# Kernel optimization log

Measured on AMD Instinct MI355X. Metric: run time of the kernel, lower is better.

## Reference

```python
import jax, jax.numpy as jnp
import numpy as np

B, NUM, TC, H = 64, 8, 64, 128
STD = 0.1


def setup_inputs() -> dict:
    key = jax.random.key(0)
    ks = jax.random.split(key, 7)
    return {
        "x": jax.random.normal(ks[0], (B, NUM, TC, H), jnp.float32),
        "att_v": jax.random.normal(ks[1], (TC, 1), jnp.float32) * STD,
        "att_w": jax.random.normal(ks[2], (H, TC), jnp.float32) * STD,
        "att_u": jax.random.normal(ks[3], (TC, TC), jnp.float32) * STD,
        "gru_kernel": jax.random.normal(ks[4], (H, 3 * H), jnp.float32) * STD,
        "gru_rkernel": jax.random.normal(ks[5], (H, 3 * H), jnp.float32) * STD,
        "gru_bias": jnp.zeros((2, 3 * H), jnp.float32),
    }


def _attention_gru(x, att_v, att_w, att_u, gru_kernel, gru_rkernel, gru_bias):
    # x: [B, num, Tc, H]. Each of the `num` attribute groups runs an independent
    # recurrence, so fold num into the batch dimension (vectorizes the outer
    # Python loop of the original).
    b, num, tc, h = x.shape
    bn = b * num
    attr = x.transpose(0, 1, 3, 2).reshape(bn, h, tc)          # [BN, H, Tc]
    # attr_input[:, i] @ u is time-invariant: hoist out of the t-loop.
    uproj = jnp.einsum('bht,ts->bhs', attr, att_u)             # [BN, H, Tc]
    v = att_v[:, 0]                                            # [Tc]
    xs = attr.transpose(2, 0, 1)                               # [Tc, BN, H]
    b_in, b_rec = gru_bias[0], gru_bias[1]                      # reset_after biases

    def step(h_state, x_col):
        # DA-RNN input attention: e_i = v^T tanh(W h + U x_i) per hidden unit i
        h_part = h_state @ att_w                               # [BN, Tc]
        e = jnp.einsum('bht,t->bh', jnp.tanh(h_part[:, None, :] + uproj), v)
        a = jax.nn.softmax(e, axis=-1)                         # [BN, H]
        x_t = x_col * a                                        # matmul-with-diag == elementwise
        # Keras GRUCell, activation=relu, recurrent_activation=sigmoid, reset_after=True
        xm = x_t @ gru_kernel + b_in                           # [BN, 3H]
        rm = h_state @ gru_rkernel + b_rec                     # [BN, 3H]
        xz, xr, xh = jnp.split(xm, 3, axis=-1)
        rz, rr, rh = jnp.split(rm, 3, axis=-1)
        z = jax.nn.sigmoid(xz + rz)
        r = jax.nn.sigmoid(xr + rr)
        hh = jax.nn.relu(xh + r * rh)
        h_new = z * h_state + (1.0 - z) * hh
        return h_new, None

    h0 = jnp.zeros((bn, h), x.dtype)
    h_final, _ = jax.lax.scan(step, h0, xs)
    return h_final.reshape(b, num, h)                          # [B, num, H]


def reference(x, att_v, att_w, att_u, gru_kernel, gru_rkernel, gru_bias):
    return _attention_gru(x, att_v, att_w, att_u, gru_kernel, gru_rkernel, gru_bias)
```

## Files before the change

kernel.cpp:

```cpp
#include <hip/hip_runtime.h>


#define OFF_ATTW  0
#define OFF_U     8192
#define OFF_XMRM  12288
#define OFF_HST   13824
#define OFF_HPP   14080
#define OFF_HPART 14592
#define OFF_XTV   14720
#define OFF_VV    14976
#define OFF_RED   15040
#define LDS_FLOATS 15056

#define FMA4(ACC, W, S) do { (ACC).x += (W).x*(S); (ACC).y += (W).y*(S); \
                             (ACC).z += (W).z*(S); (ACC).w += (W).w*(S); } while(0)

__global__ __launch_bounds__(256, 1)
void attn_gru_kernel(const float* __restrict__ x, const float* __restrict__ att_v,
                     const float* __restrict__ att_w, const float* __restrict__ att_u,
                     const float* __restrict__ gk, const float* __restrict__ grk,
                     const float* __restrict__ gbias, float* __restrict__ out) {
    __shared__ float lds[LDS_FLOATS];
    const int tid = threadIdx.x;
    const int bn0 = blockIdx.x * 2;

    for (int i = tid; i < 8192; i += 256) lds[OFF_ATTW + i] = att_w[i];
    for (int i = tid; i < 4096; i += 256) lds[OFF_U + i] = att_u[i];
    if (tid < 64) lds[OFF_VV + tid] = att_v[tid];
    lds[OFF_HST + tid] = 0.0f;
    __syncthreads();

    const int seq = tid >> 7;
    const int hh  = tid & 127;
    const int s_  = tid & 63;
    const int hg  = tid >> 6;

    float upreg[64];
    #pragma unroll
    for (int s2 = 0; s2 < 64; ++s2) upreg[s2] = 0.0f;
    {
        const float* xb = x + (size_t)(bn0 + seq) * 8192 + hh;
        for (int t = 0; t < 64; ++t) {
            float xv = xb[t * 128];
            const float* Ur = lds + OFF_U + t * 64;
            #pragma unroll
            for (int s2 = 0; s2 < 64; ++s2) upreg[s2] += xv * Ur[s2];
        }
    }

    const int col4 = tid * 4;
    const int dmat = (col4 >= 384) ? 1 : 0;
    const int dj   = col4 - dmat * 384;
    const float* Wm = (dmat ? grk : gk) + dj;
    const int ivoff = dmat ? OFF_HST : OFF_XTV;
    float4 dbias = make_float4(0.f, 0.f, 0.f, 0.f);
    if (tid < 192) dbias = *(const float4*)(gbias + dmat * 384 + dj);

    const float* xcol = x + (size_t)(bn0 + seq) * 8192 + hh;

    __syncthreads();

    for (int t = 0; t < 64; ++t) {
        float xv = xcol[t * 128];

        {
            float p0 = 0.f, p1 = 0.f;
            const float* wgl = lds + OFF_ATTW + hg * 32 * 64 + s_;
            #pragma unroll
            for (int k = 0; k < 32; ++k) {
                float w = wgl[k * 64];
                p0 += lds[OFF_HST + hg * 32 + k] * w;
                p1 += lds[OFF_HST + 128 + hg * 32 + k] * w;
            }
            lds[OFF_HPP + (0 * 4 + hg) * 64 + s_] = p0;
            lds[OFF_HPP + (1 * 4 + hg) * 64 + s_] = p1;
        }
        __syncthreads();

        if (tid < 128) {
            int sq = tid >> 6, ss = tid & 63;
            lds[OFF_HPART + sq * 64 + ss] =
                  lds[OFF_HPP + (sq * 4 + 0) * 64 + ss]
                + lds[OFF_HPP + (sq * 4 + 1) * 64 + ss]
                + lds[OFF_HPP + (sq * 4 + 2) * 64 + ss]
                + lds[OFF_HPP + (sq * 4 + 3) * 64 + ss];
        }
        __syncthreads();

        float e = 0.f;
        {
            const float* hp = lds + OFF_HPART + seq * 64;
            #pragma unroll
            for (int s2 = 0; s2 < 64; ++s2) {
                float arg = hp[s2] + upreg[s2];
                float u2 = __expf(2.0f * arg);
                float th = 1.0f - __fdividef(2.0f, u2 + 1.0f);
                e += th * lds[OFF_VV + s2];
            }
        }
        float p = __expf(e);
        float sm = p;
        #pragma unroll
        for (int off = 32; off >= 1; off >>= 1) sm += __shfl_xor(sm, off, 64);
        if ((tid & 63) == 0) lds[OFF_RED + 8 + hg] = sm;
        __syncthreads();
        float denom = lds[OFF_RED + 8 + seq * 2] + lds[OFF_RED + 8 + seq * 2 + 1];
        float a = __fdividef(p, denom);
        lds[OFF_XTV + seq * 128 + hh] = a * xv;
        __syncthreads();

        if (tid < 192) {
            float4 a0 = make_float4(0.f, 0.f, 0.f, 0.f);
            float4 a1 = make_float4(0.f, 0.f, 0.f, 0.f);
            #pragma unroll 1
            for (int c = 0; c < 4; ++c) {
                float4 w[32];
                #pragma unroll
                for (int r = 0; r < 32; ++r)
                    w[r] = *(const float4*)(Wm + (size_t)(c * 32 + r) * 384);
                const float* i0 = lds + ivoff + c * 32;
                #pragma unroll
                for (int r4 = 0; r4 < 8; ++r4) {
                    float4 iA = *(const float4*)(i0 + r4 * 4);
                    float4 iB = *(const float4*)(i0 + 128 + r4 * 4);
                    FMA4(a0, w[r4*4+0], iA.x); FMA4(a1, w[r4*4+0], iB.x);
                    FMA4(a0, w[r4*4+1], iA.y); FMA4(a1, w[r4*4+1], iB.y);
                    FMA4(a0, w[r4*4+2], iA.z); FMA4(a1, w[r4*4+2], iB.z);
                    FMA4(a0, w[r4*4+3], iA.w); FMA4(a1, w[r4*4+3], iB.w);
                }
            }
            *(float4*)(lds + OFF_XMRM + (dmat * 2 + 0) * 384 + dj) =
                make_float4(a0.x + dbias.x, a0.y + dbias.y, a0.z + dbias.z, a0.w + dbias.w);
            *(float4*)(lds + OFF_XMRM + (dmat * 2 + 1) * 384 + dj) =
                make_float4(a1.x + dbias.x, a1.y + dbias.y, a1.z + dbias.z, a1.w + dbias.w);
        }
        __syncthreads();

        {
            const float* xm = lds + OFF_XMRM + (0 * 2 + seq) * 384;
            const float* rm = lds + OFF_XMRM + (1 * 2 + seq) * 384;
            float xz = xm[hh], xr = xm[128 + hh], xh = xm[256 + hh];
            float rz = rm[hh], rr = rm[128 + hh], rh = rm[256 + hh];
            float z = __fdividef(1.0f, 1.0f + __expf(-(xz + rz)));
            float r = __fdividef(1.0f, 1.0f + __expf(-(xr + rr)));
            float hc = xh + r * rh;
            hc = hc > 0.f ? hc : 0.f;
            float hold = lds[OFF_HST + seq * 128 + hh];
            lds[OFF_HST + seq * 128 + hh] = z * hold + (1.0f - z) * hc;
        }
        __syncthreads();
    }

    out[(size_t)(bn0 + seq) * 128 + hh] = lds[OFF_HST + seq * 128 + hh];
}

extern "C" void kernel_launch(void* const* d_in, const int* in_sizes, int n_in,
                              void* d_out, int out_size, void* d_ws, size_t ws_size,
                              hipStream_t stream) {
    (void)in_sizes; (void)n_in; (void)out_size; (void)d_ws; (void)ws_size;
    const float* x      = (const float*)d_in[0];
    const float* att_v  = (const float*)d_in[1];
    const float* att_w  = (const float*)d_in[2];
    const float* att_u  = (const float*)d_in[3];
    const float* gk     = (const float*)d_in[4];
    const float* grk    = (const float*)d_in[5];
    const float* gbias  = (const float*)d_in[6];
    float* out = (float*)d_out;
    hipLaunchKernelGGL(attn_gru_kernel, dim3(256), dim3(256), 0, stream,
                       x, att_v, att_w, att_u, gk, grk, gbias, out);
}
```

Baseline: 461.7 us.

## Process four sequences per block and restructure per-step work split

Each block now handles four batch-sequences instead of two, halving the grid to 128 blocks and amortising each global load of the GRU weights over four input vectors. The GRU matvec is remapped so all 256 threads compute three output columns each (previously only 192 threads were active). The attention projection drops the partial-sum reduction stage and its barrier, with one wave computing a full h·W row per sequence. The tanh-weighted sum is rewritten algebraically as sum(v) minus twice a weighted sum of 1/(exp+1). The cost is twice as many upreg registers per thread and only half as many blocks, so fewer CUs have work on a 256-CU part.

Result: slower. 789.7 us (+71.0%).

```diff
diff --git a/kernel.cpp b/kernel.cpp
--- a/kernel.cpp
+++ b/kernel.cpp
@@ -4,16 +4,15 @@
 #define OFF_ATTW  0
 #define OFF_U     8192
 #define OFF_XMRM  12288
-#define OFF_HST   13824
-#define OFF_HPP   14080
-#define OFF_HPART 14592
-#define OFF_XTV   14720
-#define OFF_VV    14976
-#define OFF_RED   15040
-#define LDS_FLOATS 15056
+#define OFF_HST   15360
+#define OFF_HPART 15872
+#define OFF_XTV   16128
+#define OFF_VV    16640
+#define OFF_RED   16704
+#define LDS_FLOATS 22016
 
-#define FMA4(ACC, W, S) do { (ACC).x += (W).x*(S); (ACC).y += (W).y*(S); \
-                             (ACC).z += (W).z*(S); (ACC).w += (W).w*(S); } while(0)
+#define FMA3(ACC, W, S) do { (ACC).x += (W).x*(S); (ACC).y += (W).y*(S); \
+                             (ACC).z += (W).z*(S); } while(0)
 
 __global__ __launch_bounds__(256, 1)
 void attn_gru_kernel(const float* __restrict__ x, const float* __restrict__ att_v,
@@ -22,136 +21,158 @@
                      const float* __restrict__ gbias, float* __restrict__ out) {
     __shared__ float lds[LDS_FLOATS];
     const int tid = threadIdx.x;
-    const int bn0 = blockIdx.x * 2;
+    const int bn0 = blockIdx.x * 4;
 
     for (int i = tid; i < 8192; i += 256) lds[OFF_ATTW + i] = att_w[i];
     for (int i = tid; i < 4096; i += 256) lds[OFF_U + i] = att_u[i];
     if (tid < 64) lds[OFF_VV + tid] = att_v[tid];
     lds[OFF_HST + tid] = 0.0f;
+    lds[OFF_HST + 256 + tid] = 0.0f;
     __syncthreads();
 
-    const int seq = tid >> 7;
-    const int hh  = tid & 127;
-    const int s_  = tid & 63;
-    const int hg  = tid >> 6;
+    const int c2  = tid >> 7;
+    const int chh = tid & 127;
+    const int w_  = tid >> 6;
+    const int asq = w_;
+    const int as_ = tid & 63;
+    const int dmat = (tid >= 128) ? 1 : 0;
+    const int dc   = 3 * (tid & 127);
+    const float* Wm = (dmat ? grk : gk) + dc;
+    const int din   = dmat ? OFF_HST : OFF_XTV;
+    const float3 b3 = *(const float3*)(gbias + dmat * 384 + dc);
 
-    float upreg[64];
+    float up0[64], up1[64];
     #pragma unroll
-    for (int s2 = 0; s2 < 64; ++s2) upreg[s2] = 0.0f;
+    for (int s2 = 0; s2 < 64; ++s2) { up0[s2] = 0.0f; up1[s2] = 0.0f; }
     {
-        const float* xb = x + (size_t)(bn0 + seq) * 8192 + hh;
+        const float* xb0 = x + (size_t)(bn0 + c2) * 8192 + chh;
+        const float* xb1 = x + (size_t)(bn0 + c2 + 2) * 8192 + chh;
         for (int t = 0; t < 64; ++t) {
-            float xv = xb[t * 128];
+            float xv0 = xb0[t * 128];
+            float xv1 = xb1[t * 128];
             const float* Ur = lds + OFF_U + t * 64;
             #pragma unroll
-            for (int s2 = 0; s2 < 64; ++s2) upreg[s2] += xv * Ur[s2];
+            for (int s2 = 0; s2 < 64; ++s2) {
+                float u = Ur[s2];
+                up0[s2] += xv0 * u;
+                up1[s2] += xv1 * u;
+            }
         }
     }
+    float sv = 0.0f;
+    #pragma unroll
+    for (int s2 = 0; s2 < 64; ++s2) sv += lds[OFF_VV + s2];
 
-    const int col4 = tid * 4;
-    const int dmat = (col4 >= 384) ? 1 : 0;
-    const int dj   = col4 - dmat * 384;
-    const float* Wm = (dmat ? grk : gk) + dj;
-    const int ivoff = dmat ? OFF_HST : OFF_XTV;
-    float4 dbias = make_float4(0.f, 0.f, 0.f, 0.f);
-    if (tid < 192) dbias = *(const float4*)(gbias + dmat * 384 + dj);
-
-    const float* xcol = x + (size_t)(bn0 + seq) * 8192 + hh;
+    const float* xc0 = x + (size_t)(bn0 + c2) * 8192 + chh;
+    const float* xc1 = x + (size_t)(bn0 + c2 + 2) * 8192 + chh;
 
     __syncthreads();
 
     for (int t = 0; t < 64; ++t) {
-        float xv = xcol[t * 128];
+        float xv0 = xc0[t * 128];
+        float xv1 = xc1[t * 128];
 
         {
-            float p0 = 0.f, p1 = 0.f;
-            const float* wgl = lds + OFF_ATTW + hg * 32 * 64 + s_;
+            float pa = 0.0f;
+            const float4* hb4 = (const float4*)(lds + OFF_HST + asq * 128);
+            const float* wgl = lds + OFF_ATTW + as_;
             #pragma unroll
-            for (int k = 0; k < 32; ++k) {
-                float w = wgl[k * 64];
-                p0 += lds[OFF_HST + hg * 32 + k] * w;
-                p1 += lds[OFF_HST + 128 + hg * 32 + k] * w;
+            for (int k4 = 0; k4 < 32; ++k4) {
+                float4 hv = hb4[k4];
+                pa += hv.x * wgl[(k4*4+0)*64] + hv.y * wgl[(k4*4+1)*64]
+                    + hv.z * wgl[(k4*4+2)*64] + hv.w * wgl[(k4*4+3)*64];
             }
-            lds[OFF_HPP + (0 * 4 + hg) * 64 + s_] = p0;
-            lds[OFF_HPP + (1 * 4 + hg) * 64 + s_] = p1;
+            lds[OFF_HPART + asq * 64 + as_] = pa;
         }
         __syncthreads();
 
-        if (tid < 128) {
-            int sq = tid >> 6, ss = tid & 63;
-            lds[OFF_HPART + sq * 64 + ss] =
-                  lds[OFF_HPP + (sq * 4 + 0) * 64 + ss]
-                + lds[OFF_HPP + (sq * 4 + 1) * 64 + ss]
-                + lds[OFF_HPP + (sq * 4 + 2) * 64 + ss]
-                + lds[OFF_HPP + (sq * 4 + 3) * 64 + ss];
+        float den0 = 0.0f, den1 = 0.0f;
+        {
+            const float* hp0 = lds + OFF_HPART + c2 * 64;
+            const float* hp1 = lds + OFF_HPART + (c2 + 2) * 64;
+            #pragma unroll
+            for (int s2 = 0; s2 < 64; ++s2) {
+                float v = lds[OFF_VV + s2];
+                den0 += v * __fdividef(1.0f, __expf(2.0f * (hp0[s2] + up0[s2])) + 1.0f);
+                den1 += v * __fdividef(1.0f, __expf(2.0f * (hp1[s2] + up1[s2])) + 1.0f);
+            }
+        }
+        float e0 = sv - 2.0f * den0;
+        float e1 = sv - 2.0f * den1;
+        float p0 = __expf(e0);
+        float p1 = __expf(e1);
+        float ws0 = p0, ws1 = p1;
+        #pragma unroll
+        for (int off = 1; off <= 32; off <<= 1) {
+            ws0 += __shfl_xor(ws0, off);
+            ws1 += __shfl_xor(ws1, off);
+        }
+        if ((tid & 63) == 0) {
+            lds[OFF_RED + w_ * 2 + 0] = ws0;
+            lds[OFF_RED + w_ * 2 + 1] = ws1;
+        }
+        __syncthreads();
+        float d0 = lds[OFF_RED + (2 * c2) * 2 + 0] + lds[OFF_RED + (2 * c2 + 1) * 2 + 0];
+        float d1 = lds[OFF_RED + (2 * c2) * 2 + 1] + lds[OFF_RED + (2 * c2 + 1) * 2 + 1];
+        lds[OFF_XTV + c2 * 128 + chh]       = __fdividef(p0, d0) * xv0;
+        lds[OFF_XTV + (c2 + 2) * 128 + chh] = __fdividef(p1, d1) * xv1;
+        __syncthreads();
+
+        {
+            float3 acc0 = {0.f, 0.f, 0.f};
+            float3 acc1 = {0.f, 0.f, 0.f};
+            float3 acc2 = {0.f, 0.f, 0.f};
+            float3 acc3 = {0.f, 0.f, 0.f};
+            #pragma unroll 1
+            for (int c = 0; c < 8; ++c) {
+                float3 w[16];
+                #pragma unroll
+                for (int r = 0; r < 16; ++r)
+                    w[r] = *(const float3*)(Wm + (size_t)(c * 16 + r) * 384);
+                const float* ib = lds + din + c * 16;
+                #pragma unroll
+                for (int r4 = 0; r4 < 4; ++r4) {
+                    float4 i0 = *(const float4*)(ib + 0 * 128 + r4 * 4);
+                    float4 i1 = *(const float4*)(ib + 1 * 128 + r4 * 4);
+                    float4 i2 = *(const float4*)(ib + 2 * 128 + r4 * 4);
+                    float4 i3 = *(const float4*)(ib + 3 * 128 + r4 * 4);
+                    FMA3(acc0, w[r4*4+0], i0.x); FMA3(acc1, w[r4*4+0], i1.x);
+                    FMA3(acc2, w[r4*4+0], i2.x); FMA3(acc3, w[r4*4+0], i3.x);
+                    FMA3(acc0, w[r4*4+1], i0.y); FMA3(acc1, w[r4*4+1], i1.y);
+                    FMA3(acc2, w[r4*4+1], i2.y); FMA3(acc3, w[r4*4+1], i3.y);
+                    FMA3(acc0, w[r4*4+2], i0.z); FMA3(acc1, w[r4*4+2], i1.z);
+                    FMA3(acc2, w[r4*4+2], i2.z); FMA3(acc3, w[r4*4+2], i3.z);
+                    FMA3(acc0, w[r4*4+3], i0.w); FMA3(acc1, w[r4*4+3], i1.w);
+                    FMA3(acc2, w[r4*4+3], i2.w); FMA3(acc3, w[r4*4+3], i3.w);
+                }
+            }
+            float* xmb = lds + OFF_XMRM + dmat * 4 * 384 + dc;
+            *(float3*)(xmb + 0 * 384) = make_float3(acc0.x + b3.x, acc0.y + b3.y, acc0.z + b3.z);
+            *(float3*)(xmb + 1 * 384) = make_float3(acc1.x + b3.x, acc1.y + b3.y, acc1.z + b3.z);
+            *(float3*)(xmb + 2 * 384) = make_float3(acc2.x + b3.x, acc2.y + b3.y, acc2.z + b3.z);
+            *(float3*)(xmb + 3 * 384) = make_float3(acc3.x + b3.x, acc3.y + b3.y, acc3.z + b3.z);
         }
         __syncthreads();
 
-        float e = 0.f;
-        {
-            const float* hp = lds + OFF_HPART + seq * 64;
-            #pragma unroll
-            for (int s2 = 0; s2 < 64; ++s2) {
-                float arg = hp[s2] + upreg[s2];
-                float u2 = __expf(2.0f * arg);
-                float th = 1.0f - __fdividef(2.0f, u2 + 1.0f);
-                e += th * lds[OFF_VV + s2];
-            }
-        }
-        float p = __expf(e);
-        float sm = p;
         #pragma unroll
-        for (int off = 32; off >= 1; off >>= 1) sm += __shfl_xor(sm, off, 64);
-        if ((tid & 63) == 0) lds[OFF_RED + 8 + hg] = sm;
-        __syncthreads();
-        float denom = lds[OFF_RED + 8 + seq * 2] + lds[OFF_RED + 8 + seq * 2 + 1];
-        float a = __fdividef(p, denom);
-        lds[OFF_XTV + seq * 128 + hh] = a * xv;
-        __syncthreads();
-
-        if (tid < 192) {
-            float4 a0 = make_float4(0.f, 0.f, 0.f, 0.f);
-            float4 a1 = make_float4(0.f, 0.f, 0.f, 0.f);
-            #pragma unroll 1
-            for (int c = 0; c < 4; ++c) {
-                float4 w[32];
-                #pragma unroll
-                for (int r = 0; r < 32; ++r)
-                    w[r] = *(const float4*)(Wm + (size_t)(c * 32 + r) * 384);
-                const float* i0 = lds + ivoff + c * 32;
-                #pragma unroll
-                for (int r4 = 0; r4 < 8; ++r4) {
-                    float4 iA = *(const float4*)(i0 + r4 * 4);
-                    float4 iB = *(const float4*)(i0 + 128 + r4 * 4);
-                    FMA4(a0, w[r4*4+0], iA.x); FMA4(a1, w[r4*4+0], iB.x);
-                    FMA4(a0, w[r4*4+1], iA.y); FMA4(a1, w[r4*4+1], iB.y);
-                    FMA4(a0, w[r4*4+2], iA.z); FMA4(a1, w[r4*4+2], iB.z);
-                    FMA4(a0, w[r4*4+3], iA.w); FMA4(a1, w[r4*4+3], iB.w);
-                }
-            }
-            *(float4*)(lds + OFF_XMRM + (dmat * 2 + 0) * 384 + dj) =
-                make_float4(a0.x + dbias.x, a0.y + dbias.y, a0.z + dbias.z, a0.w + dbias.w);
-            *(float4*)(lds + OFF_XMRM + (dmat * 2 + 1) * 384 + dj) =
-                make_float4(a1.x + dbias.x, a1.y + dbias.y, a1.z + dbias.z, a1.w + dbias.w);
-        }
-        __syncthreads();
-
-        {
-            const float* xm = lds + OFF_XMRM + (0 * 2 + seq) * 384;
-            const float* rm = lds + OFF_XMRM + (1 * 2 + seq) * 384;
-            float xz = xm[hh], xr = xm[128 + hh], xh = xm[256 + hh];
-            float rz = rm[hh], rr = rm[128 + hh], rh = rm[256 + hh];
+        for (int j = 0; j < 2; ++j) {
+            const int sq = c2 + 2 * j;
+            const float* xm = lds + OFF_XMRM + sq * 384;
+            const float* rm = lds + OFF_XMRM + (4 + sq) * 384;
+            float xz = xm[chh], xr = xm[128 + chh], xh_ = xm[256 + chh];
+            float rz = rm[chh], rr = rm[128 + chh], rh = rm[256 + chh];
             float z = __fdividef(1.0f, 1.0f + __expf(-(xz + rz)));
             float r = __fdividef(1.0f, 1.0f + __expf(-(xr + rr)));
-            float hc = xh + r * rh;
-            hc = hc > 0.f ? hc : 0.f;
-            float hold = lds[OFF_HST + seq * 128 + hh];
-            lds[OFF_HST + seq * 128 + hh] = z * hold + (1.0f - z) * hc;
+            float hc = xh_ + r * rh;
+            hc = hc > 0.0f ? hc : 0.0f;
+            float hold = lds[OFF_HST + sq * 128 + chh];
+            lds[OFF_HST + sq * 128 + chh] = z * hold + (1.0f - z) * hc;
         }
         __syncthreads();
     }
 
-    out[(size_t)(bn0 + seq) * 128 + hh] = lds[OFF_HST + seq * 128 + hh];
+    out[(size_t)(bn0 + c2) * 128 + chh]     = lds[OFF_HST + c2 * 128 + chh];
+    out[(size_t)(bn0 + c2 + 2) * 128 + chh] = lds[OFF_HST + (c2 + 2) * 128 + chh];
 }
 
 extern "C" void kernel_launch(void* const* d_in, const int* in_sizes, int n_in,
@@ -166,6 +187,6 @@
     const float* grk    = (const float*)d_in[5];
     const float* gbias  = (const float*)d_in[6];
     float* out = (float*)d_out;
-    hipLaunchKernelGGL(attn_gru_kernel, dim3(256), dim3(256), 0, stream,
+    hipLaunchKernelGGL(attn_gru_kernel, dim3(128), dim3(256), 0, stream,
                        x, att_v, att_w, att_u, gk, grk, gbias, out);
 }
```
